# Kernel tuning notes

Measured on AMD Instinct MI355X. Metric: run time of the kernel, lower is better.

The kernel has to match this reference:

```python
import jax, jax.numpy as jnp
import numpy as np

P = 64
K = 64
D = 2048
KERNEL_MUL = 2.0
KERNEL_NUM = 5


def setup_inputs() -> dict:
    key = jax.random.key(0)
    k1, k2 = jax.random.split(key)
    source = jax.random.normal(k1, (P * K, D), dtype=jnp.float32)
    target = jax.random.normal(k2, (P * K, D), dtype=jnp.float32)
    return {"source": source, "target": target}


def _mmd_terms(source, target):
    # split into P groups of K rows each, process all splits at once
    src = source.reshape(P, K, D)
    tgt = target.reshape(P, K, D)
    total = jnp.concatenate([src, tgt], axis=1)          # [P, 2K, D]
    n = 2 * K
    # pairwise squared L2 distances per split: [P, 2K, 2K]
    sq = jnp.sum(total * total, axis=-1)                  # [P, 2K]
    gram = jnp.einsum('pid,pjd->pij', total, total)       # [P, 2K, 2K]
    l2 = sq[:, :, None] + sq[:, None, :] - 2.0 * gram
    # bandwidth from detached distances (torch uses L2_distance.data)
    bw = jax.lax.stop_gradient(jnp.sum(l2, axis=(1, 2))) / (n * n - n)  # [P]
    bw = bw / (KERNEL_MUL ** (KERNEL_NUM // 2))
    mults = KERNEL_MUL ** jnp.arange(KERNEL_NUM, dtype=jnp.float32)     # [kn]
    bws = bw[:, None] * mults[None, :] + 1e-9                           # [P, kn]
    # multi-bandwidth Gaussian kernel sum: [P, 2K, 2K]
    kern = jnp.sum(jnp.exp(-l2[:, None, :, :] / bws[:, :, None, None]), axis=1)
    XX = kern[:, :K, :K]
    YY = kern[:, K:, K:]
    XY = kern[:, :K, K:]
    YX = kern[:, K:, :K]
    xx = jnp.mean(XX, axis=(1, 2))
    yy = jnp.mean(YY, axis=(1, 2))
    xy = jnp.mean(XY, axis=(1, 2))
    yx = jnp.mean(YX, axis=(1, 2))
    per_split_loss = xx + yy - xy - yx                    # [P]
    total_loss = jnp.sum(per_split_loss) / P
    return total_loss, l2, xx, yy, xy, yx


def reference(source, target):
    total_loss, l2, xx, yy, xy, yx = _mmd_terms(source, target)
    # original returns max of l2dist from the LAST split only
    max_l2_last = jnp.max(l2[-1])
    return (total_loss.reshape(1), max_l2_last,
            jnp.sum(xx) / P, jnp.sum(yy) / P, jnp.sum(xy) / P, jnp.sum(yx) / P)
```

## Files before the change

### kernel.cpp

```cpp
#include <hip/hip_runtime.h>

typedef _Float16 half8 __attribute__((ext_vector_type(8)));
typedef _Float16 half4v __attribute__((ext_vector_type(4)));
typedef float floatx4 __attribute__((ext_vector_type(4)));
typedef unsigned int uint2v __attribute__((ext_vector_type(2)));

#define NSPLIT 64
#define KS 64
#define DIM 2048
#define NROW 128
#define BK 128
#define KSPL 4
#define KCH (DIM / KSPL)
#define NKC_A (KCH / BK)
#define SST 152
#define GSZ (NROW * NROW)
#define NBLK (NSPLIT * KSPL)
#define GT2F_OFF (NBLK * GSZ / 2)
#define PART_OFF (GT2F_OFF + NBLK)
#define FLAG_OFF (PART_OFF + 256)


__device__ __forceinline__ unsigned int pk16(float a, float b) {
  return __builtin_bit_cast(unsigned int, __builtin_amdgcn_cvt_pkrtz(a, b));
}

__global__ __launch_bounds__(1024) void fused_kernel(const float* __restrict__ src,
                                                     const float* __restrict__ tgt,
                                                     float* __restrict__ ws,
                                                     float* __restrict__ out,
                                                     unsigned nonce) {
  __shared__ __align__(16) _Float16 stage[2][NROW * SST];
  __shared__ float red[16];
  __shared__ float sqv[NROW];
  __shared__ float bcast[8];
  __shared__ float redm[16];
  __shared__ float redqA[16];
  __shared__ float redqB[16];
  __shared__ float gsum3;
  __shared__ unsigned smagic;

  const int b = blockIdx.x;
  const int p = (b & 7) | ((b >> 5) << 3);
  const int c = (b >> 3) & 3;
  const int tid = threadIdx.x;
  const int lane = tid & 63;
  const int wave = tid >> 6;

  unsigned* flag1 = (unsigned*)(ws + FLAG_OFF);
  unsigned* flag2 = flag1 + 192;
  if (tid == 0) smagic = flag1[256] ^ (2u * nonce + 1u);

  const int srow = tid >> 3;
  const int c4 = (tid & 7) * 4;
  const float* rowp = ((srow < KS) ? (src + (size_t)(p * KS + srow) * DIM)
                                   : (tgt + (size_t)(p * KS + (srow - KS)) * DIM)) +
                      c * KCH;

  const int wr = (wave >> 2) * 32;
  const int wc = (wave & 3) * 32;
  const int fr = lane & 15;
  const int fk = (lane >> 4) * 8;

  floatx4 acc00 = {0.f, 0.f, 0.f, 0.f};
  floatx4 acc01 = {0.f, 0.f, 0.f, 0.f};
  floatx4 acc10 = {0.f, 0.f, 0.f, 0.f};
  floatx4 acc11 = {0.f, 0.f, 0.f, 0.f};

  floatx4 f0, f1, f2, f3;
#define LOADK(kc)                                                   \
  do {                                                              \
    const floatx4* gp_ = (const floatx4*)(rowp + (kc)*BK + c4);     \
    f0 = __builtin_nontemporal_load(gp_);                           \
    f1 = __builtin_nontemporal_load(gp_ + 8);                       \
    f2 = __builtin_nontemporal_load(gp_ + 16);                      \
    f3 = __builtin_nontemporal_load(gp_ + 24);                      \
  } while (0)

  LOADK(0);
#pragma unroll
  for (int kc = 0; kc < NKC_A; ++kc) {
    {
      _Float16* sp = &stage[kc & 1][srow * SST + c4];
      *(uint2v*)(sp)      = (uint2v){pk16(f0[0], f0[1]), pk16(f0[2], f0[3])};
      *(uint2v*)(sp + 32) = (uint2v){pk16(f1[0], f1[1]), pk16(f1[2], f1[3])};
      *(uint2v*)(sp + 64) = (uint2v){pk16(f2[0], f2[1]), pk16(f2[2], f2[3])};
      *(uint2v*)(sp + 96) = (uint2v){pk16(f3[0], f3[1]), pk16(f3[2], f3[3])};
    }
    if (kc + 1 < NKC_A) LOADK(kc + 1);
    __syncthreads();
    const _Float16* sbuf = stage[kc & 1];
#pragma unroll
    for (int ks = 0; ks < 4; ++ks) {
      const int ko = ks * 32 + fk;
      half8 a0 = *(const half8*)&sbuf[(wr + fr) * SST + ko];
      half8 a1 = *(const half8*)&sbuf[(wr + 16 + fr) * SST + ko];
      half8 b0 = *(const half8*)&sbuf[(wc + fr) * SST + ko];
      half8 b1 = *(const half8*)&sbuf[(wc + 16 + fr) * SST + ko];
      acc00 = __builtin_amdgcn_mfma_f32_16x16x32_f16(a0, b0, acc00, 0, 0, 0);
      acc01 = __builtin_amdgcn_mfma_f32_16x16x32_f16(a0, b1, acc01, 0, 0, 0);
      acc10 = __builtin_amdgcn_mfma_f32_16x16x32_f16(a1, b0, acc10, 0, 0, 0);
      acc11 = __builtin_amdgcn_mfma_f32_16x16x32_f16(a1, b1, acc11, 0, 0, 0);
    }
  }
#undef LOADK

  half4v h0, h1, h2, h3;
#pragma unroll
  for (int r = 0; r < 4; ++r) {
    h0[r] = (_Float16)acc00[r];
    h1[r] = (_Float16)acc01[r];
    h2[r] = (_Float16)acc10[r];
    h3[r] = (_Float16)acc11[r];
  }
  if (c != 3) {
    _Float16* hs = (_Float16*)ws + (size_t)(p * KSPL + c) * GSZ + wave * 1024 + lane * 4;
    *(half4v*)(hs)       = h0;
    *(half4v*)(hs + 256) = h1;
    *(half4v*)(hs + 512) = h2;
    *(half4v*)(hs + 768) = h3;
  }

  float gsum = 0.0f;
#pragma unroll
  for (int r = 0; r < 4; ++r) gsum += acc00[r] + acc01[r] + acc10[r] + acc11[r];
#pragma unroll
  for (int m = 1; m <= 32; m <<= 1) gsum += __shfl_xor(gsum, m, 64);
  if (lane == 0) red[wave] = gsum;
  __syncthreads();

  float tot = 0.0f;
  if (tid == 0)
    for (int w = 0; w < 16; ++w) tot += red[w];

  if (c != 3) {
    if (tid == 0) {
      ws[GT2F_OFF + p * 4 + c] = tot;
      __threadfence();
      atomicExch(&flag1[p * 3 + c], smagic);
    }
    return;
  }

  if (tid == 0) gsum3 = tot;
  _Float16* lsl = (_Float16*)stage;
  {
    _Float16* ls = lsl + wave * 1024 + lane * 4;
    *(half4v*)(ls)       = h0;
    *(half4v*)(ls + 256) = h1;
    *(half4v*)(ls + 512) = h2;
    *(half4v*)(ls + 768) = h3;
  }
  const unsigned mg = smagic;
  if (tid < 3) {
    while (atomicAdd(&flag1[p * 3 + tid], 0u) != mg) __builtin_amdgcn_s_sleep(1);
  }
  __syncthreads();
  __threadfence();

  const _Float16* sb = (const _Float16*)ws + (size_t)(p * KSPL) * GSZ;

  if (tid < NROW) {
    const int i = tid;
    const int wd = (i >> 5) * 5;
    const int ad = ((i >> 4) & 1) * 3;
    const int lnd = (((i & 15) >> 2) << 4) + (i & 15);
    const int idxd = wd * 1024 + ad * 256 + lnd * 4 + (i & 3);
    float d = 0.0f;
#pragma unroll
    for (int c8 = 0; c8 < 3; ++c8) d += (float)sb[(size_t)c8 * GSZ + idxd];
    d += (float)lsl[idxd];
    sqv[i] = d;
  }
  __syncthreads();

  if (tid == 0) {
    float ssq = 0.0f;
    for (int i = 0; i < NROW; ++i) ssq += sqv[i];
    float gt = ws[GT2F_OFF + p * 4 + 0] + ws[GT2F_OFF + p * 4 + 1] +
               ws[GT2F_OFF + p * 4 + 2] + gsum3;
    float suml2 = 2.0f * (float)NROW * ssq - 2.0f * gt;
    float bw = suml2 / (float)(NROW * NROW - NROW) * 0.25f;
    float mult = 1.0f;
    for (int k = 0; k < 5; ++k) {
      bcast[k] = 1.0f / (bw * mult + 1e-9f);
      mult *= 2.0f;
    }
  }
  __syncthreads();

  const float ib0 = bcast[0], ib1 = bcast[1], ib2 = bcast[2], ib3 = bcast[3], ib4 = bcast[4];
  const int r0b = ((tid >> 7) & 1) * 16 + ((tid >> 4) & 3) * 4;
  const int col = (tid >> 8) * 32 + ((tid >> 6) & 1) * 16 + (tid & 15);
  const float sqc = sqv[col];
  float sA = 0.0f, sB = 0.0f, lmax = 0.0f;
#pragma unroll
  for (int rb2 = 0; rb2 < 4; ++rb2) {
    const int off = rb2 * 4096 + tid * 4;
    half4v a0 = *(const half4v*)(sb + off);
    half4v a1 = *(const half4v*)(sb + GSZ + off);
    half4v a2 = *(const half4v*)(sb + 2 * (size_t)GSZ + off);
    half4v a3 = *(const half4v*)(lsl + off);
    const floatx4 sr = *(const floatx4*)&sqv[rb2 * 32 + r0b];
    float qsum = 0.0f;
#pragma unroll
    for (int k = 0; k < 4; ++k) {
      float g = (float)a0[k] + (float)a1[k] + (float)a2[k] + (float)a3[k];
      float v = sr[k] + sqc - 2.0f * g;
      lmax = fmaxf(lmax, v);
      qsum += __expf(-v * ib0) + __expf(-v * ib1) + __expf(-v * ib2) +
              __expf(-v * ib3) + __expf(-v * ib4);
    }
    if (rb2 < 2) sA += qsum; else sB += qsum;
  }
#pragma unroll
  for (int m = 1; m <= 32; m <<= 1) {
    lmax = fmaxf(lmax, __shfl_xor(lmax, m, 64));
    sA += __shfl_xor(sA, m, 64);
    sB += __shfl_xor(sB, m, 64);
  }
  if (lane == 0) { redm[wave] = lmax; redqA[wave] = sA; redqB[wave] = sB; }
  __syncthreads();

  if (tid == 0) {
    float xx = 0.f, xy = 0.f, yx = 0.f, yy = 0.f, mx = 0.f;
#pragma unroll
    for (int w = 0; w < 8; ++w) { xx += redqA[w]; yx += redqB[w]; }
#pragma unroll
    for (int w = 8; w < 16; ++w) { xy += redqA[w]; yy += redqB[w]; }
#pragma unroll
    for (int w = 0; w < 16; ++w) mx = fmaxf(mx, redm[w]);
    ((float4*)(ws + PART_OFF))[p] = make_float4(xx, xy, yx, yy);
    if (p == NSPLIT - 1) out[1] = mx;
    __threadfence();
    atomicExch(&flag2[p], mg);
  }

  if (p == 0 && tid < 64) {
    while (atomicAdd(&flag2[tid], 0u) != mg) __builtin_amdgcn_s_sleep(1);
    __threadfence();
    float4 pt = ((const float4*)(ws + PART_OFF))[tid];
    float xx = pt.x, xy = pt.y, yx = pt.z, yy = pt.w;
#pragma unroll
    for (int m = 1; m <= 32; m <<= 1) {
      xx += __shfl_xor(xx, m, 64);
      xy += __shfl_xor(xy, m, 64);
      yx += __shfl_xor(yx, m, 64);
      yy += __shfl_xor(yy, m, 64);
    }
    if (tid == 0) {
      const float inv = 1.0f / (4096.0f * 64.0f);
      out[0] = (xx + yy - xy - yx) * inv;
      out[2] = xx * inv;
      out[3] = yy * inv;
      out[4] = xy * inv;
      out[5] = yx * inv;
    }
  }
}

extern "C" void kernel_launch(void* const* d_in, const int* in_sizes, int n_in,
                              void* d_out, int out_size, void* d_ws, size_t ws_size,
                              hipStream_t stream) {
  const float* src = (const float*)d_in[0];
  const float* tgt = (const float*)d_in[1];
  float* out = (float*)d_out;
  float* ws = (float*)d_ws;
  static unsigned nonce = 0;
  ++nonce;
  fused_kernel<<<NBLK, 1024, 0, stream>>>(src, tgt, ws, out, nonce);
}
```

Measured before the change: 127.8 us.

## Drop split-K across blocks; one block per split computes full Gram in registers

New measurement: 111.0 us. -13.2%, faster.

```diff
diff --git a/kernel.cpp b/kernel.cpp
--- a/kernel.cpp
+++ b/kernel.cpp
@@ -1,7 +1,6 @@
 #include <hip/hip_runtime.h>
 
 typedef _Float16 half8 __attribute__((ext_vector_type(8)));
-typedef _Float16 half4v __attribute__((ext_vector_type(4)));
 typedef float floatx4 __attribute__((ext_vector_type(4)));
 typedef unsigned int uint2v __attribute__((ext_vector_type(2)));
 
@@ -10,52 +9,41 @@
 #define DIM 2048
 #define NROW 128
 #define BK 128
-#define KSPL 4
-#define KCH (DIM / KSPL)
-#define NKC_A (KCH / BK)
+#define NPAN (DIM / BK)
 #define SST 152
-#define GSZ (NROW * NROW)
-#define NBLK (NSPLIT * KSPL)
-#define GT2F_OFF (NBLK * GSZ / 2)
-#define PART_OFF (GT2F_OFF + NBLK)
-#define FLAG_OFF (PART_OFF + 256)
+#define PART_OFF 0
+#define FLAG_OFF 256
 
 
 __device__ __forceinline__ unsigned int pk16(float a, float b) {
   return __builtin_bit_cast(unsigned int, __builtin_amdgcn_cvt_pkrtz(a, b));
 }
 
-__global__ __launch_bounds__(1024) void fused_kernel(const float* __restrict__ src,
-                                                     const float* __restrict__ tgt,
-                                                     float* __restrict__ ws,
-                                                     float* __restrict__ out,
-                                                     unsigned nonce) {
+__global__ __launch_bounds__(1024) void mmd_kernel(const float* __restrict__ src,
+                                                   const float* __restrict__ tgt,
+                                                   float* __restrict__ ws,
+                                                   float* __restrict__ out,
+                                                   unsigned nonce) {
   __shared__ __align__(16) _Float16 stage[2][NROW * SST];
   __shared__ float red[16];
   __shared__ float sqv[NROW];
   __shared__ float bcast[8];
   __shared__ float redm[16];
-  __shared__ float redqA[16];
-  __shared__ float redqB[16];
-  __shared__ float gsum3;
+  __shared__ float redq[16];
   __shared__ unsigned smagic;
 
-  const int b = blockIdx.x;
-  const int p = (b & 7) | ((b >> 5) << 3);
-  const int c = (b >> 3) & 3;
+  const int p = blockIdx.x;
   const int tid = threadIdx.x;
   const int lane = tid & 63;
   const int wave = tid >> 6;
 
-  unsigned* flag1 = (unsigned*)(ws + FLAG_OFF);
-  unsigned* flag2 = flag1 + 192;
-  if (tid == 0) smagic = flag1[256] ^ (2u * nonce + 1u);
+  unsigned* flag2 = (unsigned*)(ws + FLAG_OFF);
+  if (tid == 0) smagic = flag2[64] ^ (2u * nonce + 1u);
 
   const int srow = tid >> 3;
   const int c4 = (tid & 7) * 4;
-  const float* rowp = ((srow < KS) ? (src + (size_t)(p * KS + srow) * DIM)
-                                   : (tgt + (size_t)(p * KS + (srow - KS)) * DIM)) +
-                      c * KCH;
+  const float* rowp = (srow < KS) ? (src + (size_t)(p * KS + srow) * DIM)
+                                  : (tgt + (size_t)(p * KS + (srow - KS)) * DIM);
 
   const int wr = (wave >> 2) * 32;
   const int wc = (wave & 3) * 32;
@@ -67,58 +55,61 @@
   floatx4 acc10 = {0.f, 0.f, 0.f, 0.f};
   floatx4 acc11 = {0.f, 0.f, 0.f, 0.f};
 
-  floatx4 f0, f1, f2, f3;
-#define LOADK(kc)                                                   \
+  floatx4 fA0, fA1, fA2, fA3, fB0, fB1, fB2, fB3;
+#define LOADK(kc, F0, F1, F2, F3)                                   \
   do {                                                              \
     const floatx4* gp_ = (const floatx4*)(rowp + (kc)*BK + c4);     \
-    f0 = __builtin_nontemporal_load(gp_);                           \
-    f1 = __builtin_nontemporal_load(gp_ + 8);                       \
-    f2 = __builtin_nontemporal_load(gp_ + 16);                      \
-    f3 = __builtin_nontemporal_load(gp_ + 24);                      \
+    F0 = gp_[0]; F1 = gp_[8]; F2 = gp_[16]; F3 = gp_[24];           \
   } while (0)
-
-  LOADK(0);
-#pragma unroll
-  for (int kc = 0; kc < NKC_A; ++kc) {
-    {
-      _Float16* sp = &stage[kc & 1][srow * SST + c4];
-      *(uint2v*)(sp)      = (uint2v){pk16(f0[0], f0[1]), pk16(f0[2], f0[3])};
-      *(uint2v*)(sp + 32) = (uint2v){pk16(f1[0], f1[1]), pk16(f1[2], f1[3])};
-      *(uint2v*)(sp + 64) = (uint2v){pk16(f2[0], f2[1]), pk16(f2[2], f2[3])};
-      *(uint2v*)(sp + 96) = (uint2v){pk16(f3[0], f3[1]), pk16(f3[2], f3[3])};
-    }
-    if (kc + 1 < NKC_A) LOADK(kc + 1);
+#define STOREP(kc, F0, F1, F2, F3)                                          \
+  do {                                                                      \
+    _Float16* sp = &stage[(kc) & 1][srow * SST + c4];                       \
+    *(uint2v*)(sp)      = (uint2v){pk16(F0[0], F0[1]), pk16(F0[2], F0[3])}; \
+    *(uint2v*)(sp + 32) = (uint2v){pk16(F1[0], F1[1]), pk16(F1[2], F1[3])}; \
+    *(uint2v*)(sp + 64) = (uint2v){pk16(F2[0], F2[1]), pk16(F2[2], F2[3])}; \
+    *(uint2v*)(sp + 96) = (uint2v){pk16(F3[0], F3[1]), pk16(F3[2], F3[3])}; \
+  } while (0)
+#define MFMAP(kc)                                                            \
+  do {                                                                       \
+    const _Float16* sbuf = stage[(kc) & 1];                                  \
+    _Pragma("unroll") for (int ks = 0; ks < 4; ++ks) {                       \
+      const int ko = ks * 32 + fk;                                           \
+      half8 a0 = *(const half8*)&sbuf[(wr + fr) * SST + ko];                 \
+      half8 a1 = *(const half8*)&sbuf[(wr + 16 + fr) * SST + ko];            \
+      half8 b0 = *(const half8*)&sbuf[(wc + fr) * SST + ko];                 \
+      half8 b1 = *(const half8*)&sbuf[(wc + 16 + fr) * SST + ko];            \
+      acc00 = __builtin_amdgcn_mfma_f32_16x16x32_f16(a0, b0, acc00, 0, 0, 0);\
+      acc01 = __builtin_amdgcn_mfma_f32_16x16x32_f16(a0, b1, acc01, 0, 0, 0);\
+      acc10 = __builtin_amdgcn_mfma_f32_16x16x32_f16(a1, b0, acc10, 0, 0, 0);\
+      acc11 = __builtin_amdgcn_mfma_f32_16x16x32_f16(a1, b1, acc11, 0, 0, 0);\
+    }                                                                        \
+  } while (0)
+
+  LOADK(0, fA0, fA1, fA2, fA3);
+  LOADK(1, fB0, fB1, fB2, fB3);
+#pragma unroll
+  for (int kc2 = 0; kc2 < NPAN / 2; ++kc2) {
+    const int kc = kc2 * 2;
+    STOREP(kc, fA0, fA1, fA2, fA3);
+    if (kc + 2 < NPAN) LOADK(kc + 2, fA0, fA1, fA2, fA3);
     __syncthreads();
-    const _Float16* sbuf = stage[kc & 1];
-#pragma unroll
-    for (int ks = 0; ks < 4; ++ks) {
-      const int ko = ks * 32 + fk;
-      half8 a0 = *(const half8*)&sbuf[(wr + fr) * SST + ko];
-      half8 a1 = *(const half8*)&sbuf[(wr + 16 + fr) * SST + ko];
-      half8 b0 = *(const half8*)&sbuf[(wc + fr) * SST + ko];
-      half8 b1 = *(const half8*)&sbuf[(wc + 16 + fr) * SST + ko];
-      acc00 = __builtin_amdgcn_mfma_f32_16x16x32_f16(a0, b0, acc00, 0, 0, 0);
-      acc01 = __builtin_amdgcn_mfma_f32_16x16x32_f16(a0, b1, acc01, 0, 0, 0);
-      acc10 = __builtin_amdgcn_mfma_f32_16x16x32_f16(a1, b0, acc10, 0, 0, 0);
-      acc11 = __builtin_amdgcn_mfma_f32_16x16x32_f16(a1, b1, acc11, 0, 0, 0);
-    }
+    MFMAP(kc);
+    STOREP(kc + 1, fB0, fB1, fB2, fB3);
+    if (kc + 3 < NPAN) LOADK(kc + 3, fB0, fB1, fB2, fB3);
+    __syncthreads();
+    MFMAP(kc + 1);
   }
 #undef LOADK
-
-  half4v h0, h1, h2, h3;
-#pragma unroll
-  for (int r = 0; r < 4; ++r) {
-    h0[r] = (_Float16)acc00[r];
-    h1[r] = (_Float16)acc01[r];
-    h2[r] = (_Float16)acc10[r];
-    h3[r] = (_Float16)acc11[r];
-  }
-  if (c != 3) {
-    _Float16* hs = (_Float16*)ws + (size_t)(p * KSPL + c) * GSZ + wave * 1024 + lane * 4;
-    *(half4v*)(hs)       = h0;
-    *(half4v*)(hs + 256) = h1;
-    *(half4v*)(hs + 512) = h2;
-    *(half4v*)(hs + 768) = h3;
+#undef STOREP
+#undef MFMAP
+
+  if (wr == wc) {
+    const int q = lane >> 4;
+    if ((fr >> 2) == q) {
+      const int s = lane & 3;
+      sqv[wr + fr] = acc00[s];
+      sqv[wr + 16 + fr] = acc11[s];
+    }
   }
 
   float gsum = 0.0f;
@@ -129,56 +120,11 @@
   if (lane == 0) red[wave] = gsum;
   __syncthreads();
 
-  float tot = 0.0f;
-  if (tid == 0)
-    for (int w = 0; w < 16; ++w) tot += red[w];
-
-  if (c != 3) {
-    if (tid == 0) {
-      ws[GT2F_OFF + p * 4 + c] = tot;
-      __threadfence();
-      atomicExch(&flag1[p * 3 + c], smagic);
-    }
-    return;
-  }
-
-  if (tid == 0) gsum3 = tot;
-  _Float16* lsl = (_Float16*)stage;
-  {
-    _Float16* ls = lsl + wave * 1024 + lane * 4;
-    *(half4v*)(ls)       = h0;
-    *(half4v*)(ls + 256) = h1;
-    *(half4v*)(ls + 512) = h2;
-    *(half4v*)(ls + 768) = h3;
-  }
-  const unsigned mg = smagic;
-  if (tid < 3) {
-    while (atomicAdd(&flag1[p * 3 + tid], 0u) != mg) __builtin_amdgcn_s_sleep(1);
-  }
-  __syncthreads();
-  __threadfence();
-
-  const _Float16* sb = (const _Float16*)ws + (size_t)(p * KSPL) * GSZ;
-
-  if (tid < NROW) {
-    const int i = tid;
-    const int wd = (i >> 5) * 5;
-    const int ad = ((i >> 4) & 1) * 3;
-    const int lnd = (((i & 15) >> 2) << 4) + (i & 15);
-    const int idxd = wd * 1024 + ad * 256 + lnd * 4 + (i & 3);
-    float d = 0.0f;
-#pragma unroll
-    for (int c8 = 0; c8 < 3; ++c8) d += (float)sb[(size_t)c8 * GSZ + idxd];
-    d += (float)lsl[idxd];
-    sqv[i] = d;
-  }
-  __syncthreads();
-
   if (tid == 0) {
     float ssq = 0.0f;
     for (int i = 0; i < NROW; ++i) ssq += sqv[i];
-    float gt = ws[GT2F_OFF + p * 4 + 0] + ws[GT2F_OFF + p * 4 + 1] +
-               ws[GT2F_OFF + p * 4 + 2] + gsum3;
+    float gt = 0.0f;
+    for (int w = 0; w < 16; ++w) gt += red[w];
     float suml2 = 2.0f * (float)NROW * ssq - 2.0f * gt;
     float bw = suml2 / (float)(NROW * NROW - NROW) * 0.25f;
     float mult = 1.0f;
@@ -190,56 +136,58 @@
   __syncthreads();
 
   const float ib0 = bcast[0], ib1 = bcast[1], ib2 = bcast[2], ib3 = bcast[3], ib4 = bcast[4];
-  const int r0b = ((tid >> 7) & 1) * 16 + ((tid >> 4) & 3) * 4;
-  const int col = (tid >> 8) * 32 + ((tid >> 6) & 1) * 16 + (tid & 15);
-  const float sqc = sqv[col];
-  float sA = 0.0f, sB = 0.0f, lmax = 0.0f;
-#pragma unroll
-  for (int rb2 = 0; rb2 < 4; ++rb2) {
-    const int off = rb2 * 4096 + tid * 4;
-    half4v a0 = *(const half4v*)(sb + off);
-    half4v a1 = *(const half4v*)(sb + GSZ + off);
-    half4v a2 = *(const half4v*)(sb + 2 * (size_t)GSZ + off);
-    half4v a3 = *(const half4v*)(lsl + off);
-    const floatx4 sr = *(const floatx4*)&sqv[rb2 * 32 + r0b];
-    float qsum = 0.0f;
-#pragma unroll
-    for (int k = 0; k < 4; ++k) {
-      float g = (float)a0[k] + (float)a1[k] + (float)a2[k] + (float)a3[k];
-      float v = sr[k] + sqc - 2.0f * g;
-      lmax = fmaxf(lmax, v);
-      qsum += __expf(-v * ib0) + __expf(-v * ib1) + __expf(-v * ib2) +
-              __expf(-v * ib3) + __expf(-v * ib4);
-    }
-    if (rb2 < 2) sA += qsum; else sB += qsum;
+  const int r0 = wr + (lane >> 4) * 4;
+  const floatx4 sr0 = *(const floatx4*)&sqv[r0];
+  const floatx4 sr1 = *(const floatx4*)&sqv[r0 + 16];
+  const float sc0 = sqv[wc + fr];
+  const float sc1 = sqv[wc + 16 + fr];
+  float qsum = 0.0f, lmax = 0.0f;
+#pragma unroll
+  for (int k = 0; k < 4; ++k) {
+    const float v00 = sr0[k] + sc0 - 2.0f * acc00[k];
+    const float v01 = sr0[k] + sc1 - 2.0f * acc01[k];
+    const float v10 = sr1[k] + sc0 - 2.0f * acc10[k];
+    const float v11 = sr1[k] + sc1 - 2.0f * acc11[k];
+    lmax = fmaxf(fmaxf(lmax, fmaxf(v00, v01)), fmaxf(v10, v11));
+    qsum += __expf(-v00 * ib0) + __expf(-v00 * ib1) + __expf(-v00 * ib2) +
+            __expf(-v00 * ib3) + __expf(-v00 * ib4);
+    qsum += __expf(-v01 * ib0) + __expf(-v01 * ib1) + __expf(-v01 * ib2) +
+            __expf(-v01 * ib3) + __expf(-v01 * ib4);
+    qsum += __expf(-v10 * ib0) + __expf(-v10 * ib1) + __expf(-v10 * ib2) +
+            __expf(-v10 * ib3) + __expf(-v10 * ib4);
+    qsum += __expf(-v11 * ib0) + __expf(-v11 * ib1) + __expf(-v11 * ib2) +
+            __expf(-v11 * ib3) + __expf(-v11 * ib4);
   }
 #pragma unroll
   for (int m = 1; m <= 32; m <<= 1) {
+    qsum += __shfl_xor(qsum, m, 64);
     lmax = fmaxf(lmax, __shfl_xor(lmax, m, 64));
-    sA += __shfl_xor(sA, m, 64);
-    sB += __shfl_xor(sB, m, 64);
-  }
-  if (lane == 0) { redm[wave] = lmax; redqA[wave] = sA; redqB[wave] = sB; }
+  }
+  if (lane == 0) { redq[wave] = qsum; redm[wave] = lmax; }
   __syncthreads();
 
   if (tid == 0) {
     float xx = 0.f, xy = 0.f, yx = 0.f, yy = 0.f, mx = 0.f;
-#pragma unroll
-    for (int w = 0; w < 8; ++w) { xx += redqA[w]; yx += redqB[w]; }
-#pragma unroll
-    for (int w = 8; w < 16; ++w) { xy += redqA[w]; yy += redqB[w]; }
-#pragma unroll
-    for (int w = 0; w < 16; ++w) mx = fmaxf(mx, redm[w]);
+    for (int w = 0; w < 16; ++w) {
+      const float v = redq[w];
+      const bool rX = (w >> 2) < 2, cX = (w & 3) < 2;
+      if (rX && cX) xx += v;
+      else if (rX) xy += v;
+      else if (cX) yx += v;
+      else yy += v;
+      mx = fmaxf(mx, redm[w]);
+    }
     ((float4*)(ws + PART_OFF))[p] = make_float4(xx, xy, yx, yy);
     if (p == NSPLIT - 1) out[1] = mx;
     __threadfence();
-    atomicExch(&flag2[p], mg);
-  }
-
-  if (p == 0 && tid < 64) {
-    while (atomicAdd(&flag2[tid], 0u) != mg) __builtin_amdgcn_s_sleep(1);
+    atomicExch(&flag2[p], smagic);
+  }
+
+  if (p == 0 && wave == 0) {
+    const unsigned mg = smagic;
+    while (atomicAdd(&flag2[lane], 0u) != mg) __builtin_amdgcn_s_sleep(4);
     __threadfence();
-    float4 pt = ((const float4*)(ws + PART_OFF))[tid];
+    float4 pt = ((const float4*)(ws + PART_OFF))[lane];
     float xx = pt.x, xy = pt.y, yx = pt.z, yy = pt.w;
 #pragma unroll
     for (int m = 1; m <= 32; m <<= 1) {
@@ -248,7 +196,7 @@
       yx += __shfl_xor(yx, m, 64);
       yy += __shfl_xor(yy, m, 64);
     }
-    if (tid == 0) {
+    if (lane == 0) {
       const float inv = 1.0f / (4096.0f * 64.0f);
       out[0] = (xx + yy - xy - yx) * inv;
       out[2] = xx * inv;
@@ -268,5 +216,5 @@
   float* ws = (float*)d_ws;
   static unsigned nonce = 0;
   ++nonce;
-  fused_kernel<<<NBLK, 1024, 0, stream>>>(src, tgt, ws, out, nonce);
+  mmd_kernel<<<NSPLIT, 1024, 0, stream>>>(src, tgt, ws, out, nonce);
 }
```
